# Kernel tuning notes

Measured on AMD Instinct MI355X. Metric: run time of the kernel, lower is better.

Reference implementation:

```python
import jax, jax.numpy as jnp
import numpy as np

B, S, F, H = 16, 512, 64, 128          # batch, seq_len, price features, lstm hidden
N, GH = 1024, 64                        # graph nodes, graph hidden
FUSE, H1, H2 = 64, 32, 1                # fusion/output head dims


def setup_inputs() -> dict:
    key = jax.random.key(0)
    ks = jax.random.split(key, 24)
    s = 0.05
    inp = {
        'price_sequence': jax.random.normal(ks[0], (B, S, F), jnp.float32),
        'graph_features': jax.random.normal(ks[1], (B, N, 1), jnp.float32),
        'adjacency_mask': (jax.random.uniform(ks[2], (N, N)) > 0.5).astype(jnp.float32),
        # LSTM layer 0 (torch gate order i,f,g,o; weights stored (4H, in))
        'Wih0': jax.random.normal(ks[3], (4 * H, F), jnp.float32) * s,
        'Whh0': jax.random.normal(ks[4], (4 * H, H), jnp.float32) * s,
        'bih0': jnp.zeros((4 * H,), jnp.float32),
        'bhh0': jnp.zeros((4 * H,), jnp.float32),
        # LSTM layer 1
        'Wih1': jax.random.normal(ks[5], (4 * H, H), jnp.float32) * s,
        'Whh1': jax.random.normal(ks[6], (4 * H, H), jnp.float32) * s,
        'bih1': jnp.zeros((4 * H,), jnp.float32),
        'bhh1': jnp.zeros((4 * H,), jnp.float32),
        # graph attention: W: Linear(1, GH) no bias -> (1, GH); attention Linear(2GH,1) split
        'Wg': jax.random.normal(ks[7], (1, GH), jnp.float32) * s,
        'a_src': jax.random.normal(ks[8], (GH,), jnp.float32) * s,
        'a_dst': jax.random.normal(ks[9], (GH,), jnp.float32) * s,
        'adj_w': jax.random.normal(ks[10], (N, N), jnp.float32) * 0.1,
        # fusion + output head
        'Wf': jax.random.normal(ks[11], (H + N * GH, FUSE), jnp.float32) * 0.01,
        'bf': jnp.zeros((FUSE,), jnp.float32),
        'W1': jax.random.normal(ks[12], (FUSE, H1), jnp.float32) * s,
        'b1': jnp.zeros((H1,), jnp.float32),
        'W2': jax.random.normal(ks[13], (H1, H2), jnp.float32) * s,
        'b2': jnp.zeros((H2,), jnp.float32),
    }
    return inp


def _lstm_layer(x, Wih, Whh, bih, bhh):
    # x: (B, S, in) batch_first; returns (B, S, H)
    b = x.shape[0]
    h0 = jnp.zeros((b, Whh.shape[1]), x.dtype)
    c0 = jnp.zeros_like(h0)
    bias = bih + bhh

    def step(carry, xt):
        h, c = carry
        gates = xt @ Wih.T + h @ Whh.T + bias  # (B, 4H)
        i, f, g, o = jnp.split(gates, 4, axis=-1)
        i, f, o = jax.nn.sigmoid(i), jax.nn.sigmoid(f), jax.nn.sigmoid(o)
        g = jnp.tanh(g)
        c = f * c + i * g
        h = o * jnp.tanh(c)
        return (h, c), h

    _, ys = jax.lax.scan(step, (h0, c0), jnp.swapaxes(x, 0, 1))
    return jnp.swapaxes(ys, 0, 1)


def _graph_attention(graph_features, adjacency_mask, Wg, a_src, a_dst, adj_w):
    h = graph_features @ Wg                       # (B, N, GH)
    # Linear([h_i ; h_j]) == h_i@a_src + h_j@a_dst  (decomposed concat-attention)
    e_src = h @ a_src                              # (B, N)
    e_dst = h @ a_dst                              # (B, N)
    scores = e_src[:, :, None] + e_dst[:, None, :]  # (B, N, N)
    scores = scores * adjacency_mask[None]
    scores = scores * jax.nn.sigmoid(adj_w)[None]
    attn = jax.nn.softmax(scores, axis=-1)
    updated = attn @ h                             # (B, N, GH)
    return updated, attn


def reference(price_sequence, graph_features, adjacency_mask,
              Wih0, Whh0, bih0, bhh0, Wih1, Whh1, bih1, bhh1,
              Wg, a_src, a_dst, adj_w, Wf, bf, W1, b1, W2, b2):
    # 2-layer LSTM (eval mode: inter-layer dropout is identity)
    y0 = _lstm_layer(price_sequence, Wih0, Whh0, bih0, bhh0)
    y1 = _lstm_layer(y0, Wih1, Whh1, bih1, bhh1)
    price_repr = y1[:, -1, :]                      # (B, H)

    graph_repr, attn = _graph_attention(graph_features, adjacency_mask, Wg, a_src, a_dst, adj_w)
    graph_flat = graph_repr.reshape(graph_repr.shape[0], -1)  # (B, N*GH)

    combined = jnp.concatenate([price_repr, graph_flat], axis=1)
    fused = jax.nn.relu(combined @ Wf + bf)
    hidden = jax.nn.relu(fused @ W1 + b1)          # head dropout is identity in eval
    predictions = (hidden @ W2 + b2).squeeze(-1)   # (B,)
    return predictions, attn
```

## Files before the change

kernel.cpp:

```cpp
#include <hip/hip_runtime.h>

typedef unsigned int u32;
typedef unsigned long long u64;
typedef _Float16 f16;
typedef _Float16 f16x8 __attribute__((ext_vector_type(8)));
typedef float f32x4 __attribute__((ext_vector_type(4)));

#define DEV __device__ __forceinline__
#define PINA(x) asm volatile("" : "+a"(x))

constexpr size_t O_XG0   = 0;
constexpr size_t O_W0HI  = O_XG0   + 16ull*512*512*4;
constexpr size_t O_W0LO  = O_W0HI  + 512ull*128*2;
constexpr size_t O_WIHHI = O_W0LO  + 512ull*128*2;
constexpr size_t O_WIHLO = O_WIHHI + 512ull*128*2;
constexpr size_t O_WHHHI = O_WIHLO + 512ull*128*2;
constexpr size_t O_WHHLO = O_WHHHI + 512ull*128*2;
constexpr size_t O_B1P   = O_WHHLO + 512ull*128*2;
constexpr size_t O_MSIG  = O_B1P   + 512*4;
constexpr size_t O_ESC   = O_MSIG  + 1024ull*1024*4;
constexpr size_t O_EDST  = O_ESC   + 16384*4;
constexpr size_t O_SBUF  = O_EDST  + 16384*4;
constexpr size_t O_PREPR = O_SBUF  + 16384*4;
constexpr size_t O_WFG   = O_PREPR + 2048*4;
constexpr size_t O_H0HI  = O_WFG   + 65536ull*4;
constexpr size_t O_H0LO  = O_H0HI  + 513ull*16*64*4;
constexpr size_t O_P1    = O_H0LO  + 513ull*16*64*4;

struct U128 { u64 x, y; };
DEV f16x8 asf16x8(u64 a, u64 b){ U128 t; t.x=a; t.y=b; return __builtin_bit_cast(f16x8, t); }
DEV u32 f16bits(f16 v){ return (u32)__builtin_bit_cast(unsigned short, v); }

DEV float sigm(float x){ x = fminf(fmaxf(x,-30.f),30.f); return __builtin_amdgcn_rcpf(1.f + __expf(-x)); }
DEV float tanh_(float x){ x = fminf(fmaxf(x,-15.f),15.f); float t = __expf(2.f*x); return (t-1.f)*__builtin_amdgcn_rcpf(t+1.f); }

DEV void bar_lds(){
  asm volatile("s_waitcnt lgkmcnt(0)" ::: "memory");
  __builtin_amdgcn_s_barrier();
  __builtin_amdgcn_sched_barrier(0);
}

__global__ __launch_bounds__(256) void k_setup(
    const float* __restrict__ price, const float* __restrict__ gf,
    const float* __restrict__ amask, const float* __restrict__ Wih0,
    const float* __restrict__ Whh0, const float* __restrict__ bih0, const float* __restrict__ bhh0,
    const float* __restrict__ Wih1, const float* __restrict__ Whh1,
    const float* __restrict__ bih1, const float* __restrict__ bhh1,
    const float* __restrict__ Wg, const float* __restrict__ a_src, const float* __restrict__ a_dst,
    const float* __restrict__ adj_w, const float* __restrict__ Wf,
    char* __restrict__ ws)
{
  const int tid = threadIdx.x;
  const int jb = blockIdx.x;
  __shared__ float P[16][64];
  __shared__ float Wt[64][128];

  if (jb < 2048) {
    const int tt = jb >> 2, p0 = (jb & 3) * 128;
    float* XG = (float*)(ws + O_XG0);
    { int idx = tid*4; int b = idx>>6, k = idx&63;
      f32x4 v = *(const f32x4*)(price + ((size_t)b*512 + tt)*64 + k);
      *(f32x4*)&P[b][k] = v; }
    { int c = tid>>1, kh = (tid&1)*32;
      int p = p0 + c; int row = (p&3)*128 + (p>>2);
      const float* src = Wih0 + row*64 + kh;
      #pragma unroll
      for (int kk=0; kk<32; kk+=4){ f32x4 v = *(const f32x4*)(src+kk);
        Wt[kh+kk+0][c]=v[0]; Wt[kh+kk+1][c]=v[1]; Wt[kh+kk+2][c]=v[2]; Wt[kh+kk+3][c]=v[3]; } }
    __syncthreads();
    { int c = tid & 127, hh2 = tid >> 7;
      int p = p0 + c; int row = (p&3)*128 + (p>>2);
      float bias = bih0[row] + bhh0[row];
      float acc[8];
      #pragma unroll
      for (int r2=0;r2<8;r2++) acc[r2] = bias;
      for (int k=0;k<64;k++){ float w = Wt[k][c];
        #pragma unroll
        for (int r2=0;r2<8;r2++) acc[r2] += w * P[hh2*8+r2][k]; }
      #pragma unroll
      for (int r2=0;r2<8;r2++)
        XG[((size_t)(hh2*8+r2)*512 + tt)*512 + p0 + c] = acc[r2]; }
  } else if (jb < 3072) {
    int idx = ((jb-2048)<<10) + tid*4;
    float* MS = (float*)(ws + O_MSIG);
    f32x4 m = *(const f32x4*)(amask+idx); f32x4 a = *(const f32x4*)(adj_w+idx);
    f32x4 o;
    #pragma unroll
    for (int e=0;e<4;e++) o[e] = m[e] * (1.f/(1.f+expf(-a[e])));
    *(f32x4*)(MS+idx) = o;
  } else if (jb < 3136) {
    unsigned short* HI = (unsigned short*)(ws+O_W0HI);
    unsigned short* LO = (unsigned short*)(ws+O_W0LO);
    int base = ((jb-3072)*256 + tid)*4;
    #pragma unroll
    for (int e=0;e<4;e++){ int idx = base+e; int p = idx>>7, k = idx&127;
      int row = (p&3)*128 + (p>>2);
      float w = Whh0[row*128 + k];
      f16 hi = (f16)w; f16 lo = (f16)((w - (float)hi)*4096.f);
      HI[idx] = (unsigned short)f16bits(hi); LO[idx] = (unsigned short)f16bits(lo); }
  } else if (jb < 3200) {
    unsigned short* HI = (unsigned short*)(ws+O_WIHHI);
    unsigned short* LO = (unsigned short*)(ws+O_WIHLO);
    int base = ((jb-3136)*256 + tid)*4;
    #pragma unroll
    for (int e=0;e<4;e++){ int idx = base+e; int p = idx>>7, k = idx&127;
      int row = (p&3)*128 + (p>>2);
      float w = Wih1[row*128 + k];
      f16 hi = (f16)w; f16 lo = (f16)((w - (float)hi)*4096.f);
      HI[idx] = (unsigned short)f16bits(hi); LO[idx] = (unsigned short)f16bits(lo); }
  } else if (jb < 3264) {
    unsigned short* HI = (unsigned short*)(ws+O_WHHHI);
    unsigned short* LO = (unsigned short*)(ws+O_WHHLO);
    int base = ((jb-3200)*256 + tid)*4;
    #pragma unroll
    for (int e=0;e<4;e++){ int idx = base+e; int p = idx>>7, k = idx&127;
      int row = (p&3)*128 + (p>>2);
      float w = Whh1[row*128 + k];
      f16 hi = (f16)w; f16 lo = (f16)((w - (float)hi)*4096.f);
      HI[idx] = (unsigned short)f16bits(hi); LO[idx] = (unsigned short)f16bits(lo); }
  } else if (jb < 3265) {
    float* B1 = (float*)(ws+O_B1P);
    for (int p = tid; p < 512; p += 256){ int row = (p&3)*128 + (p>>2); B1[p] = bih1[row]+bhh1[row]; }
  } else if (jb < 3281) {
    float cs = 0.f, cd = 0.f;
    for (int g=0; g<64; g++){ cs += Wg[g]*a_src[g]; cd += Wg[g]*a_dst[g]; }
    float* ESC = (float*)(ws+O_ESC); float* EDS = (float*)(ws+O_EDST);
    int base = (jb-3265)*1024 + tid*4;
    f32x4 g4 = *(const f32x4*)(gf+base);
    f32x4 e1, e2;
    #pragma unroll
    for (int e=0;e<4;e++){ e1[e] = g4[e]*cs; e2[e] = g4[e]*cd; }
    *(f32x4*)(ESC+base) = e1; *(f32x4*)(EDS+base) = e2;
  } else {
    float* WFG = (float*)(ws+O_WFG);
    int n = (jb-3281)*4 + (tid>>6); int f = tid & 63;
    float acc = 0.f;
    for (int g=0; g<64; g++) acc += Wg[g] * Wf[((size_t)(128 + n*64 + g))*64 + f];
    WFG[n*64 + f] = acc;
  }
}

struct SM3 { u32 hbuf[2][1024]; };

template<int LAYER>
DEV void rnn3(char* __restrict__ ws, int bg, int tid, SM3* sm)
{
  const int lane = tid & 63, w = tid >> 6;
  const int r = lane & 15, q = lane >> 4;
  const int j = w*16 + r;
  const int b0 = bg*8 + 2*q;

  const u64* WHI = (const u64*)(ws + (LAYER ? O_WHHHI : O_W0HI));
  const u64* WLO = (const u64*)(ws + (LAYER ? O_WHHLO : O_W0LO));
  f16x8 Bhi[4][4], Blo[4][4];
  #pragma unroll
  for (int t=0;t<4;t++)
    #pragma unroll
    for (int ks=0;ks<4;ks++){
      int o = (4*j + t)*32 + ks*8 + q*2;
      Bhi[t][ks] = asf16x8(WHI[o], WHI[o+1]);
      Blo[t][ks] = asf16x8(WLO[o], WLO[o+1]);
    }
  #pragma unroll
  for (int t=0;t<4;t++)
    #pragma unroll
    for (int ks=0;ks<4;ks++){ PINA(Bhi[t][ks]); PINA(Blo[t][ks]); }

  u32* H0HIp = (u32*)(ws+O_H0HI);
  u32* H0LOp = (u32*)(ws+O_H0LO);
  const float* P1f = (const float*)(ws+O_P1);
  const float* XG  = (const float*)(ws+O_XG0);

  for (int idx = tid; idx < 2*1024; idx += 512) ((u32*)sm->hbuf)[idx] = 0u;

  f32x4 ac[2], aN[2], aNN[2];
  #pragma unroll
  for (int d=0; d<2; ++d){
    if constexpr (!LAYER) {
      ac[d] = *(const f32x4*)(XG + ((size_t)((b0+d)*512 + 0))*512 + 4*j);
      aN[d] = *(const f32x4*)(XG + ((size_t)((b0+d)*512 + 1))*512 + 4*j);
    } else {
      ac[d] = *(const f32x4*)(P1f + ((size_t)(1*16 + b0+d))*512 + 4*j);
      aN[d] = *(const f32x4*)(P1f + ((size_t)(2*16 + b0+d))*512 + 4*j);
    }
    aNN[d] = ac[d];
  }
  float cst[2] = {0.f, 0.f};
  int cur = 0;
  __syncthreads();

  for (int s=1; s<=512; ++s){
    { int sp = (s<=510) ? (s+2) : 512;
      #pragma unroll
      for (int d=0; d<2; ++d){
        if constexpr (!LAYER)
          aNN[d] = *(const f32x4*)(XG + ((size_t)((b0+d)*512 + sp-1))*512 + 4*j);
        else
          aNN[d] = *(const f32x4*)(P1f + ((size_t)(sp*16 + b0+d))*512 + 4*j);
      } }

    f32x4 accA[4], accB[4];
    #pragma unroll
    for (int t=0;t<4;t++){ accA[t]=f32x4{0,0,0,0}; accB[t]=f32x4{0,0,0,0}; }
    #pragma unroll
    for (int ks=0;ks<4;ks++){
      f16x8 av = *(const f16x8*)&sm->hbuf[cur][ks*256 + lane*4];
      #pragma unroll
      for (int t=0;t<4;t++){
        accA[t] = __builtin_amdgcn_mfma_f32_16x16x32_f16(av, Bhi[t][ks], accA[t], 0,0,0);
        accB[t] = __builtin_amdgcn_mfma_f32_16x16x32_f16(av, Blo[t][ks], accB[t], 0,0,0);
      }
    }

    float hv[2];
    #pragma unroll
    for (int d=0; d<2; ++d){
      float g0 = accA[0][2*d] + (accA[0][2*d+1] + accB[0][2*d])*(1.f/4096.f);
      float g1 = accA[1][2*d] + (accA[1][2*d+1] + accB[1][2*d])*(1.f/4096.f);
      float g2 = accA[2][2*d] + (accA[2][2*d+1] + accB[2][2*d])*(1.f/4096.f);
      float g3 = accA[3][2*d] + (accA[3][2*d+1] + accB[3][2*d])*(1.f/4096.f);
      float I = sigm(g0 + ac[d][0]);
      float F = sigm(g1 + ac[d][1]);
      float G = tanh_(g2 + ac[d][2]);
      float O = sigm(g3 + ac[d][3]);
      cst[d] = F*cst[d] + I*G;
      hv[d] = O * tanh_(cst[d]);
    }

    u32 hp[2], lp[2];
    #pragma unroll
    for (int d=0; d<2; ++d){
      f16 hh = (f16)hv[d]; f16 hl = (f16)((hv[d] - (float)hh)*4096.f);
      u32 hb = f16bits(hh), lb = f16bits(hl);
      u32 oh = (u32)__shfl_xor((int)hb, 1, 64);
      u32 ol = (u32)__shfl_xor((int)lb, 1, 64);
      hp[d] = hb | (oh<<16); lp[d] = lb | (ol<<16);
    }
    int nxt = cur^1;
    if ((r & 1) == 0){
      const int cp = w*8 + (r>>1);
      const int wbase = (cp>>4)*256 + ((cp>>2)&3)*64 + 16*q + (cp&3);
      u32* hb8 = sm->hbuf[nxt];
      hb8[wbase+ 0] = hp[0];
      hb8[wbase+ 4] = lp[0];
      hb8[wbase+ 8] = hp[1];
      hb8[wbase+12] = lp[1];
      if constexpr (!LAYER){
        const int cpo = cp;
        H0HIp[(s*16 + b0  )*64 + cpo] = hp[0];
        H0LOp[(s*16 + b0  )*64 + cpo] = lp[0];
        H0HIp[(s*16 + b0+1)*64 + cpo] = hp[1];
        H0LOp[(s*16 + b0+1)*64 + cpo] = lp[1];
      }
    }
    if constexpr (LAYER){
      if (s == 512){
        ((float*)(ws+O_PREPR))[(b0  )*128 + j] = hv[0];
        ((float*)(ws+O_PREPR))[(b0+1)*128 + j] = hv[1];
      }
    }

    bar_lds();

    cur = nxt;
    #pragma unroll
    for (int d=0; d<2; ++d){ ac[d] = aN[d]; aN[d] = aNN[d]; }
  }
}

__global__
__attribute__((amdgpu_flat_work_group_size(512,512), amdgpu_waves_per_eu(2,2)))
void k_lstm0(char* __restrict__ ws)
{
  __shared__ SM3 sm;
  rnn3<0>(ws, blockIdx.x, threadIdx.x, &sm);
}

__global__
__attribute__((amdgpu_flat_work_group_size(512,512), amdgpu_waves_per_eu(2,2)))
void k_lstm1(char* __restrict__ ws)
{
  __shared__ SM3 sm;
  rnn3<1>(ws, blockIdx.x, threadIdx.x, &sm);
}

__global__ __launch_bounds__(512) void k_gemm1(char* __restrict__ ws)
{
  const int tid = threadIdx.x;
  const int lane = tid & 63, w = tid >> 6;
  const int c = lane & 15, q = lane >> 4;
  const int s = blockIdx.x + 1;

  const u64* WHI = (const u64*)(ws+O_WIHHI);
  const u64* WLO = (const u64*)(ws+O_WIHLO);
  f16x8 Bhi[4][4], Blo[4][4];
  #pragma unroll
  for (int t=0;t<4;t++)
    #pragma unroll
    for (int ks=0;ks<4;ks++){
      int o = (w*64 + t*16 + c)*32 + ks*8 + q*2;
      Bhi[t][ks] = asf16x8(WHI[o], WHI[o+1]);
      Blo[t][ks] = asf16x8(WLO[o], WLO[o+1]);
    }
  float bias_t[4];
  #pragma unroll
  for (int t=0;t<4;t++) bias_t[t] = ((const float*)(ws+O_B1P))[w*64 + t*16 + c];

  const u64* H0HIu = (const u64*)(ws+O_H0HI);
  const u64* H0LOu = (const u64*)(ws+O_H0LO);
  float* P1f = (float*)(ws+O_P1);

  u64 AH[4][2], AL[4][2];
  #pragma unroll
  for (int ks=0;ks<4;ks++){
    size_t o = ((size_t)(s*16 + c))*32 + ks*8 + q*2;
    AH[ks][0]=H0HIu[o]; AH[ks][1]=H0HIu[o+1];
    AL[ks][0]=H0LOu[o]; AL[ks][1]=H0LOu[o+1];
  }
  f32x4 acc[4], accl[4];
  #pragma unroll
  for (int t=0;t<4;t++){ acc[t]=f32x4{0,0,0,0}; accl[t]=f32x4{0,0,0,0}; }
  #pragma unroll
  for (int ks=0;ks<4;ks++){
    f16x8 ah  = asf16x8(AH[ks][0], AH[ks][1]);
    f16x8 al_ = asf16x8(AL[ks][0], AL[ks][1]);
    #pragma unroll
    for (int t=0;t<4;t++){
      acc[t]  = __builtin_amdgcn_mfma_f32_16x16x32_f16(ah,  Bhi[t][ks], acc[t],  0,0,0);
      accl[t] = __builtin_amdgcn_mfma_f32_16x16x32_f16(ah,  Blo[t][ks], accl[t], 0,0,0);
      accl[t] = __builtin_amdgcn_mfma_f32_16x16x32_f16(al_, Bhi[t][ks], accl[t], 0,0,0);
    }
  }
  #pragma unroll
  for (int t=0;t<4;t++){
    #pragma unroll
    for (int i=0;i<4;i++){
      float v = acc[t][i] + accl[t][i]*(1.f/4096.f) + bias_t[t];
      P1f[((size_t)(s*16 + q*4 + i))*512 + w*64 + t*16 + c] = v;
    }
  }
}

DEV float wredMax(float v){
  #pragma unroll
  for (int o=32;o;o>>=1) v = fmaxf(v, __shfl_xor(v,o,64));
  return v;
}
DEV float wredSum(float v){
  #pragma unroll
  for (int o=32;o;o>>=1) v += __shfl_xor(v,o,64);
  return v;
}

__global__ __launch_bounds__(512) void k_attn(const float* __restrict__ gf,
                                              char* __restrict__ ws, float* __restrict__ out)
{
  __shared__ float red[8];
  const int tid = threadIdx.x;
  const int row = blockIdx.x;
  const int b = row >> 10, i = row & 1023;
  const int w = tid >> 6;
  const float* MSIG = (const float*)(ws+O_MSIG);
  const float* ESC  = (const float*)(ws+O_ESC);
  const float* EDST = (const float*)(ws+O_EDST);
  float* SBUF = (float*)(ws+O_SBUF);

  const float ei = ESC[(b<<10)+i];
  float pv[2];
  float mx = -3.4e38f;
  #pragma unroll
  for (int k2=0;k2<2;k2++){
    int jj = tid + (k2<<9);
    float sc = (ei + EDST[(b<<10)+jj]) * MSIG[((size_t)i<<10)+jj];
    pv[k2] = sc; mx = fmaxf(mx, sc);
  }
  mx = wredMax(mx);
  if ((tid&63)==0) red[w] = mx;
  __syncthreads();
  mx = fmaxf(fmaxf(fmaxf(red[0],red[1]),fmaxf(red[2],red[3])),
             fmaxf(fmaxf(red[4],red[5]),fmaxf(red[6],red[7])));
  __syncthreads();

  float sum = 0.f;
  #pragma unroll
  for (int k2=0;k2<2;k2++){ pv[k2] = __expf(pv[k2]-mx); sum += pv[k2]; }
  sum = wredSum(sum);
  if ((tid&63)==0) red[w] = sum;
  __syncthreads();
  sum = red[0]+red[1]+red[2]+red[3]+red[4]+red[5]+red[6]+red[7];
  __syncthreads();

  const float rinv = 1.0f / sum;
  float sacc = 0.f;
  const size_t obase = 16 + ((size_t)row << 10);
  #pragma unroll
  for (int k2=0;k2<2;k2++){
    int jj = tid + (k2<<9);
    float a = pv[k2]*rinv;
    out[obase + jj] = a;
    sacc += a * gf[(b<<10)+jj];
  }
  sacc = wredSum(sacc);
  if ((tid&63)==0) red[w] = sacc;
  __syncthreads();
  if (tid==0) SBUF[row] = red[0]+red[1]+red[2]+red[3]+red[4]+red[5]+red[6]+red[7];
}

__global__ __launch_bounds__(256) void k_mlp(const float* __restrict__ Wf, const float* __restrict__ bf,
  const float* __restrict__ W1, const float* __restrict__ b1,
  const float* __restrict__ W2, const float* __restrict__ b2,
  const char* __restrict__ ws, float* __restrict__ out)
{
  __shared__ float sS[1024];
  __shared__ float sP[128];
  __shared__ float sR[256];
  __shared__ float sF[96];
  const int b = blockIdx.x, tid = threadIdx.x;
  const float* SBUF = (const float*)(ws+O_SBUF);
  const float* PREPR= (const float*)(ws+O_PREPR);
  const float* WFG  = (const float*)(ws+O_WFG);

  { f32x4 v = *(const f32x4*)(SBUF + (b<<10) + tid*4); *(f32x4*)&sS[tid*4] = v; }
  if (tid < 128) sP[tid] = PREPR[b*128 + tid];
  __syncthreads();

  const int f = tid & 63, kq = tid >> 6;
  float acc = 0.f;
  for (int n = kq*256; n < kq*256+256; ++n) acc += sS[n] * WFG[n*64 + f];
  if (kq == 0) {
    for (int k=0;k<128;k++) acc += sP[k] * Wf[k*64 + f];
    acc += bf[f];
  }
  sR[tid] = acc; __syncthreads();
  if (tid < 64) {
    float v = sR[tid] + sR[tid+64] + sR[tid+128] + sR[tid+192];
    sF[tid] = fmaxf(v, 0.f);
  }
  __syncthreads();
  if (tid < 32) {
    float a = 0.f;
    for (int k=0;k<64;k++) a += sF[k] * W1[k*32 + tid];
    sF[64+tid] = fmaxf(a + b1[tid], 0.f);
  }
  __syncthreads();
  if (tid == 0) {
    float a = 0.f;
    for (int k=0;k<32;k++) a += sF[64+k] * W2[k];
    out[b] = a + b2[0];
  }
}

extern "C" void kernel_launch(void* const* d_in, const int* in_sizes, int n_in,
                              void* d_out, int out_size, void* d_ws, size_t ws_size,
                              hipStream_t stream)
{
  const float* price = (const float*)d_in[0];
  const float* gf    = (const float*)d_in[1];
  const float* amask = (const float*)d_in[2];
  const float* Wih0  = (const float*)d_in[3];
  const float* Whh0  = (const float*)d_in[4];
  const float* bih0  = (const float*)d_in[5];
  const float* bhh0  = (const float*)d_in[6];
  const float* Wih1  = (const float*)d_in[7];
  const float* Whh1  = (const float*)d_in[8];
  const float* bih1  = (const float*)d_in[9];
  const float* bhh1  = (const float*)d_in[10];
  const float* Wg    = (const float*)d_in[11];
  const float* asrc  = (const float*)d_in[12];
  const float* adst  = (const float*)d_in[13];
  const float* adjw  = (const float*)d_in[14];
  const float* Wf    = (const float*)d_in[15];
  const float* bf    = (const float*)d_in[16];
  const float* W1    = (const float*)d_in[17];
  const float* b1    = (const float*)d_in[18];
  const float* W2    = (const float*)d_in[19];
  const float* b2    = (const float*)d_in[20];
  char* ws = (char*)d_ws;
  float* out = (float*)d_out;

  k_setup<<<dim3(3537), dim3(256), 0, stream>>>(price, gf, amask, Wih0, Whh0, bih0, bhh0,
                                                Wih1, Whh1, bih1, bhh1, Wg, asrc, adst, adjw, Wf, ws);
  k_attn<<<dim3(16384), dim3(512), 0, stream>>>(gf, ws, out);
  k_lstm0<<<dim3(2), dim3(512), 0, stream>>>(ws);
  k_gemm1<<<dim3(512), dim3(512), 0, stream>>>(ws);
  k_lstm1<<<dim3(2), dim3(512), 0, stream>>>(ws);
  k_mlp<<<dim3(16), dim3(256), 0, stream>>>(Wf, bf, W1, b1, W2, b2, (const char*)ws, out);
}
```

Baseline: 1.415 ms.

## Pipeline LSTM layers and input GEMM in one persistent kernel with flags

Merges the layer-0 LSTM, the layer-1 input projection GEMM and the layer-1 LSTM into one six-block kernel. Blocks hand off per-timestep data through global memory guarded by atomic flag spins, so layer 1 runs a few steps behind layer 0 instead of waiting for it to finish. This targets the serial latency of running two 512-step recurrences back to back. In exchange it relies on all six blocks being resident at the same time, adds spin-wait and atomic overheads, and the spin has a bounded timeout that could proceed with stale data if a producer stalls.

```diff
diff --git a/kernel.cpp b/kernel.cpp
--- a/kernel.cpp
+++ b/kernel.cpp
@@ -7,6 +7,7 @@
 typedef float f32x4 __attribute__((ext_vector_type(4)));
 
 #define DEV __device__ __forceinline__
+#define SCP __HIP_MEMORY_SCOPE_AGENT
 #define PINA(x) asm volatile("" : "+a"(x))
 
 constexpr size_t O_XG0   = 0;
@@ -26,13 +27,24 @@
 constexpr size_t O_H0HI  = O_WFG   + 65536ull*4;
 constexpr size_t O_H0LO  = O_H0HI  + 513ull*16*64*4;
 constexpr size_t O_P1    = O_H0LO  + 513ull*16*64*4;
+constexpr size_t O_FLG0  = O_P1    + 513ull*16*512*4;
+constexpr size_t O_FLGP  = O_FLG0  + 513ull*2*4;
 
 struct U128 { u64 x, y; };
 DEV f16x8 asf16x8(u64 a, u64 b){ U128 t; t.x=a; t.y=b; return __builtin_bit_cast(f16x8, t); }
+DEV f32x4 asf32x4(u64 a, u64 b){ U128 t; t.x=a; t.y=b; return __builtin_bit_cast(f32x4, t); }
 DEV u32 f16bits(f16 v){ return (u32)__builtin_bit_cast(unsigned short, v); }
 
 DEV float sigm(float x){ x = fminf(fmaxf(x,-30.f),30.f); return __builtin_amdgcn_rcpf(1.f + __expf(-x)); }
 DEV float tanh_(float x){ x = fminf(fmaxf(x,-15.f),15.f); float t = __expf(2.f*x); return (t-1.f)*__builtin_amdgcn_rcpf(t+1.f); }
+
+DEV u32 FV(int s){ return 0x5AB00000u + (u32)s; }
+
+DEV void spin1(const u32* p, u32 tv){
+  int gd = 1<<18;
+  while (__hip_atomic_load(p,__ATOMIC_RELAXED,SCP)!=tv && --gd){}
+  (void)__hip_atomic_load(p,__ATOMIC_ACQUIRE,SCP);
+}
 
 DEV void bar_lds(){
   asm volatile("s_waitcnt lgkmcnt(0)" ::: "memory");
@@ -143,7 +155,7 @@
 struct SM3 { u32 hbuf[2][1024]; };
 
 template<int LAYER>
-DEV void rnn3(char* __restrict__ ws, int bg, int tid, SM3* sm)
+DEV void rnn_pipe(char* __restrict__ ws, int bg, int tid, SM3* sm)
 {
   const int lane = tid & 63, w = tid >> 6;
   const int r = lane & 15, q = lane >> 4;
@@ -168,36 +180,54 @@
 
   u32* H0HIp = (u32*)(ws+O_H0HI);
   u32* H0LOp = (u32*)(ws+O_H0LO);
-  const float* P1f = (const float*)(ws+O_P1);
+  const u64* P1u = (const u64*)(ws+O_P1);
   const float* XG  = (const float*)(ws+O_XG0);
+  u32* FLG0p = (u32*)(ws+O_FLG0);
+  const u32* FLGPp = (const u32*)(ws+O_FLGP);
 
   for (int idx = tid; idx < 2*1024; idx += 512) ((u32*)sm->hbuf)[idx] = 0u;
 
-  f32x4 ac[2], aN[2], aNN[2];
+  f32x4 xc[2], xN[2], xNN[2];
+  u64 pc[2][2], pn[2][2], pnn[2][2];
   #pragma unroll
   for (int d=0; d<2; ++d){
-    if constexpr (!LAYER) {
-      ac[d] = *(const f32x4*)(XG + ((size_t)((b0+d)*512 + 0))*512 + 4*j);
-      aN[d] = *(const f32x4*)(XG + ((size_t)((b0+d)*512 + 1))*512 + 4*j);
-    } else {
-      ac[d] = *(const f32x4*)(P1f + ((size_t)(1*16 + b0+d))*512 + 4*j);
-      aN[d] = *(const f32x4*)(P1f + ((size_t)(2*16 + b0+d))*512 + 4*j);
-    }
-    aNN[d] = ac[d];
+    xc[d]=f32x4{0,0,0,0}; xN[d]=f32x4{0,0,0,0}; xNN[d]=f32x4{0,0,0,0};
+    pc[d][0]=pc[d][1]=pn[d][0]=pn[d][1]=pnn[d][0]=pnn[d][1]=0;
+  }
+  if constexpr (!LAYER) {
+    #pragma unroll
+    for (int d=0; d<2; ++d){
+      xc[d] = *(const f32x4*)(XG + ((size_t)((b0+d)*512 + 0))*512 + 4*j);
+      xN[d] = *(const f32x4*)(XG + ((size_t)((b0+d)*512 + 1))*512 + 4*j);
+    }
+  } else {
+    spin1(FLGPp + 1*2 + bg, FV(1));
+    #pragma unroll
+    for (int d=0; d<2; ++d){
+      size_t o = ((size_t)(1*16 + b0+d)*512 + 4*j) >> 1;
+      pc[d][0] = __hip_atomic_load(P1u+o,   __ATOMIC_RELAXED, SCP);
+      pc[d][1] = __hip_atomic_load(P1u+o+1, __ATOMIC_RELAXED, SCP);
+    }
+    spin1(FLGPp + 2*2 + bg, FV(2));
+    #pragma unroll
+    for (int d=0; d<2; ++d){
+      size_t o = ((size_t)(2*16 + b0+d)*512 + 4*j) >> 1;
+      pn[d][0] = __hip_atomic_load(P1u+o,   __ATOMIC_RELAXED, SCP);
+      pn[d][1] = __hip_atomic_load(P1u+o+1, __ATOMIC_RELAXED, SCP);
+    }
   }
   float cst[2] = {0.f, 0.f};
   int cur = 0;
   __syncthreads();
 
   for (int s=1; s<=512; ++s){
-    { int sp = (s<=510) ? (s+2) : 512;
-      #pragma unroll
-      for (int d=0; d<2; ++d){
-        if constexpr (!LAYER)
-          aNN[d] = *(const f32x4*)(XG + ((size_t)((b0+d)*512 + sp-1))*512 + 4*j);
-        else
-          aNN[d] = *(const f32x4*)(P1f + ((size_t)(sp*16 + b0+d))*512 + 4*j);
-      } }
+    if constexpr (!LAYER) {
+      int sp = (s<=510) ? (s+2) : 512;
+      #pragma unroll
+      for (int d=0; d<2; ++d)
+        xNN[d] = *(const f32x4*)(XG + ((size_t)((b0+d)*512 + sp-1))*512 + 4*j);
+      __builtin_amdgcn_sched_barrier(0);
+    }
 
     f32x4 accA[4], accB[4];
     #pragma unroll
@@ -209,6 +239,17 @@
       for (int t=0;t<4;t++){
         accA[t] = __builtin_amdgcn_mfma_f32_16x16x32_f16(av, Bhi[t][ks], accA[t], 0,0,0);
         accB[t] = __builtin_amdgcn_mfma_f32_16x16x32_f16(av, Blo[t][ks], accB[t], 0,0,0);
+      }
+    }
+
+    if constexpr (LAYER) {
+      int sp = (s+2 <= 512) ? (s+2) : 512;
+      if (s+2 <= 512) spin1(FLGPp + sp*2 + bg, FV(sp));
+      #pragma unroll
+      for (int d=0; d<2; ++d){
+        size_t o = ((size_t)(sp*16 + b0+d)*512 + 4*j) >> 1;
+        pnn[d][0] = __hip_atomic_load(P1u+o,   __ATOMIC_RELAXED, SCP);
+        pnn[d][1] = __hip_atomic_load(P1u+o+1, __ATOMIC_RELAXED, SCP);
       }
     }
 
@@ -219,10 +260,11 @@
       float g1 = accA[1][2*d] + (accA[1][2*d+1] + accB[1][2*d])*(1.f/4096.f);
       float g2 = accA[2][2*d] + (accA[2][2*d+1] + accB[2][2*d])*(1.f/4096.f);
       float g3 = accA[3][2*d] + (accA[3][2*d+1] + accB[3][2*d])*(1.f/4096.f);
-      float I = sigm(g0 + ac[d][0]);
-      float F = sigm(g1 + ac[d][1]);
-      float G = tanh_(g2 + ac[d][2]);
-      float O = sigm(g3 + ac[d][3]);
+      f32x4 add = LAYER ? asf32x4(pc[d][0],pc[d][1]) : xc[d];
+      float I = sigm(g0 + add[0]);
+      float F = sigm(g1 + add[1]);
+      float G = tanh_(g2 + add[2]);
+      float O = sigm(g3 + add[3]);
       cst[d] = F*cst[d] + I*G;
       hv[d] = O * tanh_(cst[d]);
     }
@@ -246,11 +288,10 @@
       hb8[wbase+ 8] = hp[1];
       hb8[wbase+12] = lp[1];
       if constexpr (!LAYER){
-        const int cpo = cp;
-        H0HIp[(s*16 + b0  )*64 + cpo] = hp[0];
-        H0LOp[(s*16 + b0  )*64 + cpo] = lp[0];
-        H0HIp[(s*16 + b0+1)*64 + cpo] = hp[1];
-        H0LOp[(s*16 + b0+1)*64 + cpo] = lp[1];
+        __hip_atomic_store(H0HIp + (s*16 + b0  )*64 + cp, hp[0], __ATOMIC_RELAXED, SCP);
+        __hip_atomic_store(H0LOp + (s*16 + b0  )*64 + cp, lp[0], __ATOMIC_RELAXED, SCP);
+        __hip_atomic_store(H0HIp + (s*16 + b0+1)*64 + cp, hp[1], __ATOMIC_RELAXED, SCP);
+        __hip_atomic_store(H0LOp + (s*16 + b0+1)*64 + cp, lp[1], __ATOMIC_RELAXED, SCP);
       }
     }
     if constexpr (LAYER){
@@ -260,36 +301,40 @@
       }
     }
 
-    bar_lds();
+    if constexpr (!LAYER){
+      __builtin_amdgcn_sched_barrier(0);
+      asm volatile("s_waitcnt vmcnt(4) lgkmcnt(0)" ::: "memory");
+      __builtin_amdgcn_s_barrier();
+      __builtin_amdgcn_sched_barrier(0);
+      if (s>=2 && tid==0)
+        __hip_atomic_store(FLG0p + (s-1)*2 + bg, FV(s-1), __ATOMIC_RELAXED, SCP);
+    } else {
+      bar_lds();
+    }
 
     cur = nxt;
     #pragma unroll
-    for (int d=0; d<2; ++d){ ac[d] = aN[d]; aN[d] = aNN[d]; }
-  }
-}
-
-__global__
-__attribute__((amdgpu_flat_work_group_size(512,512), amdgpu_waves_per_eu(2,2)))
-void k_lstm0(char* __restrict__ ws)
-{
-  __shared__ SM3 sm;
-  rnn3<0>(ws, blockIdx.x, threadIdx.x, &sm);
-}
-
-__global__
-__attribute__((amdgpu_flat_work_group_size(512,512), amdgpu_waves_per_eu(2,2)))
-void k_lstm1(char* __restrict__ ws)
-{
-  __shared__ SM3 sm;
-  rnn3<1>(ws, blockIdx.x, threadIdx.x, &sm);
-}
-
-__global__ __launch_bounds__(512) void k_gemm1(char* __restrict__ ws)
-{
-  const int tid = threadIdx.x;
+    for (int d=0; d<2; ++d){
+      xc[d]=xN[d]; xN[d]=xNN[d];
+      pc[d][0]=pn[d][0]; pc[d][1]=pn[d][1];
+      pn[d][0]=pnn[d][0]; pn[d][1]=pnn[d][1];
+    }
+  }
+
+  if constexpr (!LAYER){
+    asm volatile("s_waitcnt vmcnt(0)" ::: "memory");
+    __syncthreads();
+    if (tid==0) __hip_atomic_store(FLG0p + 512*2 + bg, FV(512), __ATOMIC_RELAXED, SCP);
+  }
+}
+
+DEV void gemm_pipe(char* __restrict__ ws, int g, int tid)
+{
   const int lane = tid & 63, w = tid >> 6;
-  const int c = lane & 15, q = lane >> 4;
-  const int s = blockIdx.x + 1;
+  const int r = lane & 15, q = lane >> 4;
+  const int jj = w*16 + r;
+  const int m = lane & 15;
+  const int bb = g*8 + (m>>1);
 
   const u64* WHI = (const u64*)(ws+O_WIHHI);
   const u64* WLO = (const u64*)(ws+O_WIHLO);
@@ -298,47 +343,70 @@
   for (int t=0;t<4;t++)
     #pragma unroll
     for (int ks=0;ks<4;ks++){
-      int o = (w*64 + t*16 + c)*32 + ks*8 + q*2;
+      int o = (4*jj + t)*32 + ks*8 + q*2;
       Bhi[t][ks] = asf16x8(WHI[o], WHI[o+1]);
       Blo[t][ks] = asf16x8(WLO[o], WLO[o+1]);
     }
+  #pragma unroll
+  for (int t=0;t<4;t++)
+    #pragma unroll
+    for (int ks=0;ks<4;ks++){ PINA(Bhi[t][ks]); PINA(Blo[t][ks]); }
+
   float bias_t[4];
   #pragma unroll
-  for (int t=0;t<4;t++) bias_t[t] = ((const float*)(ws+O_B1P))[w*64 + t*16 + c];
-
-  const u64* H0HIu = (const u64*)(ws+O_H0HI);
-  const u64* H0LOu = (const u64*)(ws+O_H0LO);
+  for (int t=0;t<4;t++) bias_t[t] = ((const float*)(ws+O_B1P))[4*jj + t];
+
+  const u64* Hsel = (const u64*)(ws + ((m&1) ? O_H0LO : O_H0HI));
   float* P1f = (float*)(ws+O_P1);
-
-  u64 AH[4][2], AL[4][2];
-  #pragma unroll
-  for (int ks=0;ks<4;ks++){
-    size_t o = ((size_t)(s*16 + c))*32 + ks*8 + q*2;
-    AH[ks][0]=H0HIu[o]; AH[ks][1]=H0HIu[o+1];
-    AL[ks][0]=H0LOu[o]; AL[ks][1]=H0LOu[o+1];
-  }
-  f32x4 acc[4], accl[4];
-  #pragma unroll
-  for (int t=0;t<4;t++){ acc[t]=f32x4{0,0,0,0}; accl[t]=f32x4{0,0,0,0}; }
-  #pragma unroll
-  for (int ks=0;ks<4;ks++){
-    f16x8 ah  = asf16x8(AH[ks][0], AH[ks][1]);
-    f16x8 al_ = asf16x8(AL[ks][0], AL[ks][1]);
+  const u32* FLG0p = (const u32*)(ws+O_FLG0);
+  u32* FLGPp = (u32*)(ws+O_FLGP);
+
+  for (int s=1; s<=512; ++s){
+    spin1(FLG0p + s*2 + g, FV(s));
+
+    u64 A[4][2];
+    #pragma unroll
+    for (int ks=0;ks<4;ks++){
+      size_t o = ((size_t)(s*16 + bb))*32 + ks*8 + q*2;
+      A[ks][0] = __hip_atomic_load(Hsel+o,   __ATOMIC_RELAXED, SCP);
+      A[ks][1] = __hip_atomic_load(Hsel+o+1, __ATOMIC_RELAXED, SCP);
+    }
+    f32x4 accA[4], accB[4];
+    #pragma unroll
+    for (int t=0;t<4;t++){ accA[t]=f32x4{0,0,0,0}; accB[t]=f32x4{0,0,0,0}; }
+    #pragma unroll
+    for (int ks=0;ks<4;ks++){
+      f16x8 av = asf16x8(A[ks][0], A[ks][1]);
+      #pragma unroll
+      for (int t=0;t<4;t++){
+        accA[t] = __builtin_amdgcn_mfma_f32_16x16x32_f16(av, Bhi[t][ks], accA[t], 0,0,0);
+        accB[t] = __builtin_amdgcn_mfma_f32_16x16x32_f16(av, Blo[t][ks], accB[t], 0,0,0);
+      }
+    }
     #pragma unroll
     for (int t=0;t<4;t++){
-      acc[t]  = __builtin_amdgcn_mfma_f32_16x16x32_f16(ah,  Bhi[t][ks], acc[t],  0,0,0);
-      accl[t] = __builtin_amdgcn_mfma_f32_16x16x32_f16(ah,  Blo[t][ks], accl[t], 0,0,0);
-      accl[t] = __builtin_amdgcn_mfma_f32_16x16x32_f16(al_, Bhi[t][ks], accl[t], 0,0,0);
-    }
-  }
-  #pragma unroll
-  for (int t=0;t<4;t++){
-    #pragma unroll
-    for (int i=0;i<4;i++){
-      float v = acc[t][i] + accl[t][i]*(1.f/4096.f) + bias_t[t];
-      P1f[((size_t)(s*16 + q*4 + i))*512 + w*64 + t*16 + c] = v;
-    }
-  }
+      #pragma unroll
+      for (int d=0; d<2; ++d){
+        float v = accA[t][2*d] + (accA[t][2*d+1] + accB[t][2*d])*(1.f/4096.f) + bias_t[t];
+        __hip_atomic_store(P1f + ((size_t)(s*16 + g*8 + 2*q + d))*512 + 4*jj + t,
+                           v, __ATOMIC_RELAXED, SCP);
+      }
+    }
+    __syncthreads();
+    if (tid==0) __hip_atomic_store(FLGPp + s*2 + g, FV(s), __ATOMIC_RELAXED, SCP);
+  }
+}
+
+__global__
+__attribute__((amdgpu_flat_work_group_size(512,512), amdgpu_waves_per_eu(2,2)))
+void k_main(char* __restrict__ ws)
+{
+  __shared__ SM3 sm;
+  const int tid = threadIdx.x;
+  const int bid = blockIdx.x;
+  if (bid < 2)      rnn_pipe<0>(ws, bid,   tid, &sm);
+  else if (bid < 4) gemm_pipe  (ws, bid-2, tid);
+  else              rnn_pipe<1>(ws, bid-4, tid, &sm);
 }
 
 DEV float wredMax(float v){
@@ -481,8 +549,6 @@
   k_setup<<<dim3(3537), dim3(256), 0, stream>>>(price, gf, amask, Wih0, Whh0, bih0, bhh0,
                                                 Wih1, Whh1, bih1, bhh1, Wg, asrc, adst, adjw, Wf, ws);
   k_attn<<<dim3(16384), dim3(512), 0, stream>>>(gf, ws, out);
-  k_lstm0<<<dim3(2), dim3(512), 0, stream>>>(ws);
-  k_gemm1<<<dim3(512), dim3(512), 0, stream>>>(ws);
-  k_lstm1<<<dim3(2), dim3(512), 0, stream>>>(ws);
+  k_main<<<dim3(6), dim3(512), 0, stream>>>(ws);
   k_mlp<<<dim3(16), dim3(256), 0, stream>>>(Wf, bf, W1, b1, W2, b2, (const char*)ws, out);
 }
```

Result: slower. 2.078 ms (+46.9%).
